# Performance work log

Measured on AMD Instinct MI355X. Metric: run time of the kernel, lower is better.

## Reference

```python
import jax, jax.numpy as jnp
import numpy as np

N_NODES = 100000


def _mean_agg(x, src, dst, n_nodes):
    # mean of src-node features over in-edges of each dst node (DGL copy_u + mean)
    summed = jax.ops.segment_sum(x[src], dst, num_segments=n_nodes)  # [N, F]
    deg = jax.ops.segment_sum(jnp.ones_like(src, dtype=x.dtype), dst, num_segments=n_nodes)
    return summed / jnp.maximum(deg, 1.0)[:, None]  # nodes w/o in-edges -> 0


def _sage_conv(x, src, dst, W_self, W_neigh, b):
    # DGL SAGEConv('mean'): fc_self(h) + fc_neigh(mean_neigh(h)) + bias
    h_neigh = _mean_agg(x, src, dst, x.shape[0])
    return x @ W_self + h_neigh @ W_neigh + b


def setup_inputs() -> dict:
    key = jax.random.key(0)
    ks = jax.random.split(key, 8)
    F_IN, F_H, E = 128, 128, 1600000
    s = 1.0 / np.sqrt(F_IN)
    return {
        "x": jax.random.normal(ks[0], (N_NODES, F_IN), dtype=jnp.float32),
        "src": jax.random.randint(ks[1], (E,), 0, N_NODES, dtype=jnp.int64),
        "dst": jax.random.randint(ks[2], (E,), 0, N_NODES, dtype=jnp.int64),
        "W1_self": jax.random.normal(ks[3], (F_IN, F_H), dtype=jnp.float32) * s,
        "W1_neigh": jax.random.normal(ks[4], (F_IN, F_H), dtype=jnp.float32) * s,
        "b1": jnp.zeros((F_H,), dtype=jnp.float32),
        "W2_self": jax.random.normal(ks[5], (F_H, F_H), dtype=jnp.float32) * s,
        "W2_neigh": jax.random.normal(ks[6], (F_H, F_H), dtype=jnp.float32) * s,
        "b2": jnp.zeros((F_H,), dtype=jnp.float32),
    }


def reference(x, src, dst, W1_self, W1_neigh, b1, W2_self, W2_neigh, b2):
    h = _sage_conv(x, src, dst, W1_self, W1_neigh, b1)
    # dropout in eval mode == identity
    h = jax.nn.relu(h)
    return _sage_conv(h, src, dst, W2_self, W2_neigh, b2)
```

## Files before the change

### kernel.cpp

```cpp
#include <hip/hip_runtime.h>

#define F 128
#define NN 100000
#define NBUK 782
#define NBLK 256
#define LD 136
#define N4 (NN * F / 4)
#define N4A (N4 / 2)
#define SORT_CAP 8192

typedef __attribute__((ext_vector_type(8))) short short8;
typedef __attribute__((ext_vector_type(4))) float f32x4;
typedef __attribute__((ext_vector_type(4))) int int4v;
typedef __attribute__((ext_vector_type(4))) unsigned short us4;
typedef unsigned short ushort_t;

__device__ __forceinline__ ushort_t f2b(float f) {
    union { float f; unsigned u; } x;
    x.f = f;
    unsigned r = x.u + 0x7fffu + ((x.u >> 16) & 1u);
    return (ushort_t)(r >> 16);
}
__device__ __forceinline__ float b2f(ushort_t u) {
    union { unsigned u; float f; } x;
    x.u = ((unsigned)u) << 16;
    return x.f;
}

__device__ __forceinline__ int4v ld_row16(const ushort_t* p) {
    int4v r;
    asm volatile("global_load_dwordx4 %0, %1, off" : "=v"(r) : "v"(p) : "memory");
    return r;
}

__global__ __launch_bounds__(256) void k1_fused(
    const int* __restrict__ dst, int* __restrict__ H, int E, int chunk,
    const float* __restrict__ Wa, const float* __restrict__ Wb,
    const float* __restrict__ Wc, const float* __restrict__ Wd,
    ushort_t* __restrict__ Oa, ushort_t* __restrict__ Ob,
    ushort_t* __restrict__ Oc, ushort_t* __restrict__ Od,
    const float* __restrict__ X, ushort_t* __restrict__ Y) {
    __shared__ union {
        int h[NBUK];
        float tile[32][33];
    } u;
    const int blk = blockIdx.x;
    if (blk < NBLK) {
        for (int i = threadIdx.x; i < NBUK; i += 256) u.h[i] = 0;
        __syncthreads();
        const int s0 = blk * chunk, s1 = min(E, s0 + chunk);
        for (int i = s0 + threadIdx.x; i < s1; i += 256)
            atomicAdd(&u.h[dst[i] >> 7], 1);
        __syncthreads();
        for (int i = threadIdx.x; i < NBUK; i += 256)
            H[blk * NBUK + i] = u.h[i];
    } else if (blk < NBLK + 64) {
        const int m = (blk - NBLK) >> 4;
        const int b = (blk - NBLK) & 15;
        const float* W = (m == 0) ? Wa : (m == 1) ? Wb : (m == 2) ? Wc : Wd;
        ushort_t* WT = (m == 0) ? Oa : (m == 1) ? Ob : (m == 2) ? Oc : Od;
        const int by = (b >> 2) * 32;
        const int bx = (b & 3) * 32;
        const int tx = threadIdx.x & 31, ty = threadIdx.x >> 5;
        for (int i = 0; i < 32; i += 8)
            u.tile[ty + i][tx] = W[(by + ty + i) * F + bx + tx];
        __syncthreads();
        for (int i = 0; i < 32; i += 8)
            WT[(bx + ty + i) * F + by + tx] = f2b(u.tile[tx][ty + i]);
    } else {
        const int i = (blk - NBLK - 64) * 256 + threadIdx.x;
        if (i < N4A) {
            float4 v = ((const float4*)X)[i];
            us4 o;
            o.x = f2b(v.x); o.y = f2b(v.y); o.z = f2b(v.z); o.w = f2b(v.w);
            ((us4*)Y)[i] = o;
        }
    }
}

__global__ __launch_bounds__(256) void scan_cols(int* __restrict__ H,
                                                 int* __restrict__ Htot) {
    __shared__ int s[NBLK];
    const int k = blockIdx.x;
    const int t = threadIdx.x;
    const int v = H[t * NBUK + k];
    s[t] = v;
    __syncthreads();
    for (int d = 1; d < NBLK; d <<= 1) {
        const int u = (t >= d) ? s[t - d] : 0;
        __syncthreads();
        s[t] += u;
        __syncthreads();
    }
    H[t * NBUK + k] = s[t] - v;
    if (t == NBLK - 1) Htot[k] = s[t];
}

__global__ __launch_bounds__(1024) void k2_fused(
    const int* __restrict__ Htot, int* __restrict__ boffs, int E,
    const float* __restrict__ X, ushort_t* __restrict__ Y) {
    if (blockIdx.x == 0) {
        __shared__ int tot[1024];
        const int k = threadIdx.x;
        const int v = (k < NBUK) ? Htot[k] : 0;
        tot[k] = v;
        __syncthreads();
        for (int d = 1; d < 1024; d <<= 1) {
            const int u = (k >= d) ? tot[k - d] : 0;
            __syncthreads();
            tot[k] += u;
            __syncthreads();
        }
        if (k < NBUK) boffs[k] = tot[k] - v;
        if (k == 0) boffs[NBUK] = E;
    } else {
        const int i = N4A + (blockIdx.x - 1) * 1024 + threadIdx.x;
        if (i < N4) {
            float4 v = ((const float4*)X)[i];
            us4 o;
            o.x = f2b(v.x); o.y = f2b(v.y); o.z = f2b(v.z); o.w = f2b(v.w);
            ((us4*)Y)[i] = o;
        }
    }
}

__global__ __launch_bounds__(256) void scatter2(const int* __restrict__ src,
                                                const int* __restrict__ dst,
                                                const int* __restrict__ H,
                                                const int* __restrict__ boffs,
                                                unsigned* __restrict__ pairs,
                                                int E, int chunk) {
    __shared__ int cur[NBUK];
    const int b = blockIdx.x;
    for (int i = threadIdx.x; i < NBUK; i += 256)
        cur[i] = boffs[i] + H[b * NBUK + i];
    __syncthreads();
    const int s0 = b * chunk, s1 = min(E, s0 + chunk);
    for (int i = s0 + threadIdx.x; i < s1; i += 256) {
        const int d = dst[i];
        const int p = atomicAdd(&cur[d >> 7], 1);
        pairs[p] = ((unsigned)(d & 127) << 20) | (unsigned)src[i];
    }
}

__global__ __launch_bounds__(256) void bucket_sort(const unsigned* __restrict__ pairs,
                                                   const int* __restrict__ boffs,
                                                   int* __restrict__ offs,
                                                   int* __restrict__ csr) {
    __shared__ int cnt[128], loffs[128], lcur[128];
    __shared__ unsigned sbuf[SORT_CAP];
    const int b = blockIdx.x, t = threadIdx.x;
    const int e0 = boffs[b], e1 = boffs[b + 1];
    const int n = e1 - e0;
    const int node0 = b << 7;
    const int nnode = min(128, NN - node0);
    if (t < 128) cnt[t] = 0;
    __syncthreads();
    for (int i = e0 + t; i < e1; i += 256) atomicAdd(&cnt[pairs[i] >> 20], 1);
    __syncthreads();
    if (t < 128) loffs[t] = cnt[t];
    __syncthreads();
    for (int d = 1; d < 128; d <<= 1) {
        int u = (t >= d && t < 128) ? loffs[t - d] : 0;
        __syncthreads();
        if (t < 128) loffs[t] += u;
        __syncthreads();
    }
    if (t < 128) {
        const int ex = loffs[t] - cnt[t];
        lcur[t] = ex;
        if (t < nnode) offs[node0 + t] = e0 + ex;
    }
    if (b == NBUK - 1 && t == 0) offs[NN] = e1;
    __syncthreads();

    if (n <= SORT_CAP) {
        for (int i = e0 + t; i < e1; i += 256) {
            const unsigned v = pairs[i];
            const int p = atomicAdd(&lcur[v >> 20], 1);
            sbuf[p] = v;
        }
        __syncthreads();
        for (int i = t; i < n; i += 256) {
            const unsigned v = sbuf[i];
            const int d = v >> 20;
            const int hi = loffs[d];
            const int lo = hi - cnt[d];
            int r = lo;
            for (int j = lo; j < hi; ++j) {
                const unsigned w = sbuf[j];
                r += (w < v) || (w == v && j < i);
            }
            csr[e0 + r] = (int)(v & 0xFFFFFu);
        }
    } else {
        for (int i = e0 + t; i < e1; i += 256) {
            const unsigned v = pairs[i];
            const int p = atomicAdd(&lcur[v >> 20], 1);
            csr[e0 + p] = (int)(v & 0xFFFFFu);
        }
    }
}

template <typename TOUT>
__global__ __launch_bounds__(256) void sage_layer(
    const ushort_t* __restrict__ Xg,
    const int* __restrict__ offs, const int* __restrict__ csr,
    const ushort_t* __restrict__ WTs, const ushort_t* __restrict__ WTn,
    const float* __restrict__ bias,
    TOUT* __restrict__ out, int relu) {
    __shared__ __align__(16) ushort_t sX[32 * LD];
    __shared__ __align__(16) ushort_t sH[32 * LD];
    const int t = threadIdx.x;
    const int lane = t & 63;
    const int wave = t >> 6;
    const int brow0 = blockIdx.x * 32;

    {
        const ushort_t* base = Xg + (size_t)brow0 * F;
        for (int i = t; i < 32 * 16; i += 256) {
            int row = i >> 4, ch = i & 15;
            *(short8*)&sX[row * LD + ch * 8] = *(const short8*)&base[row * F + ch * 8];
        }
    }

    {
        const int slot = lane >> 4;
        const int cl = lane & 15;
        const int c8 = cl * 8;
#pragma unroll
        for (int rr = 0; rr < 2; rr++) {
            const int rloc = wave * 8 + slot * 2 + rr;
            const int row = brow0 + rloc;
            const int e0 = offs[row], e1 = offs[row + 1];
            const int d = e1 - e0;
            float acc[8];
#pragma unroll
            for (int j = 0; j < 8; j++) acc[j] = 0.f;
            if (d > 0) {
                const int e1m1 = e1 - 1;
                const int nb = (d + 7) >> 3;
#pragma unroll 1
                for (int b = 0; b < nb; b++) {
                    const int e = e0 + b * 8;
                    const int i0 = csr[e];
                    const int i1 = csr[min(e + 1, e1m1)];
                    const int i2 = csr[min(e + 2, e1m1)];
                    const int i3 = csr[min(e + 3, e1m1)];
                    const int i4 = csr[min(e + 4, e1m1)];
                    const int i5 = csr[min(e + 5, e1m1)];
                    const int i6 = csr[min(e + 6, e1m1)];
                    const int i7 = csr[min(e + 7, e1m1)];
                    int4v r0 = ld_row16(Xg + (size_t)i0 * F + c8);
                    int4v r1 = ld_row16(Xg + (size_t)i1 * F + c8);
                    int4v r2 = ld_row16(Xg + (size_t)i2 * F + c8);
                    int4v r3 = ld_row16(Xg + (size_t)i3 * F + c8);
                    int4v r4 = ld_row16(Xg + (size_t)i4 * F + c8);
                    int4v r5 = ld_row16(Xg + (size_t)i5 * F + c8);
                    int4v r6 = ld_row16(Xg + (size_t)i6 * F + c8);
                    int4v r7 = ld_row16(Xg + (size_t)i7 * F + c8);
                    asm volatile("s_waitcnt vmcnt(0)" ::: "memory");
                    asm volatile("" : "+v"(r0), "+v"(r1), "+v"(r2), "+v"(r3),
                                       "+v"(r4), "+v"(r5), "+v"(r6), "+v"(r7));
                    __builtin_amdgcn_sched_barrier(0);
                    const short8 v0 = __builtin_bit_cast(short8, r0);
                    const short8 v1 = __builtin_bit_cast(short8, r1);
                    const short8 v2 = __builtin_bit_cast(short8, r2);
                    const short8 v3 = __builtin_bit_cast(short8, r3);
                    const short8 v4 = __builtin_bit_cast(short8, r4);
                    const short8 v5 = __builtin_bit_cast(short8, r5);
                    const short8 v6 = __builtin_bit_cast(short8, r6);
                    const short8 v7 = __builtin_bit_cast(short8, r7);
                    const float m1 = (e + 1 < e1) ? 1.f : 0.f;
                    const float m2 = (e + 2 < e1) ? 1.f : 0.f;
                    const float m3 = (e + 3 < e1) ? 1.f : 0.f;
                    const float m4 = (e + 4 < e1) ? 1.f : 0.f;
                    const float m5 = (e + 5 < e1) ? 1.f : 0.f;
                    const float m6 = (e + 6 < e1) ? 1.f : 0.f;
                    const float m7 = (e + 7 < e1) ? 1.f : 0.f;
#pragma unroll
                    for (int j = 0; j < 8; j++) {
                        float s01 = b2f((ushort_t)v0[j]) + m1 * b2f((ushort_t)v1[j]);
                        float s23 = m2 * b2f((ushort_t)v2[j]) + m3 * b2f((ushort_t)v3[j]);
                        float s45 = m4 * b2f((ushort_t)v4[j]) + m5 * b2f((ushort_t)v5[j]);
                        float s67 = m6 * b2f((ushort_t)v6[j]) + m7 * b2f((ushort_t)v7[j]);
                        acc[j] += (s01 + s23) + (s45 + s67);
                    }
                }
            }
            const float inv = (d > 0) ? (1.0f / (float)d) : 0.f;
            short8 o;
#pragma unroll
            for (int j = 0; j < 8; j++) o[j] = (short)f2b(acc[j] * inv);
            *(short8*)&sH[rloc * LD + c8] = o;
        }
    }
    __syncthreads();

    const int q = lane >> 4, nl = lane & 15;
    const int colbase = wave * 32;
    f32x4 acc00 = (f32x4)0.f, acc01 = (f32x4)0.f, acc10 = (f32x4)0.f, acc11 = (f32x4)0.f;
#pragma unroll
    for (int ks = 0; ks < 4; ks++) {
        const int ko = ks * 32 + q * 8;
        const short8 aS0 = *(const short8*)&sX[nl * LD + ko];
        const short8 aS1 = *(const short8*)&sX[(16 + nl) * LD + ko];
        const short8 aN0 = *(const short8*)&sH[nl * LD + ko];
        const short8 aN1 = *(const short8*)&sH[(16 + nl) * LD + ko];
        const size_t bo0 = (size_t)(colbase + nl) * F + ko;
        const size_t bo1 = (size_t)(colbase + 16 + nl) * F + ko;
        const short8 bS0 = *(const short8*)&WTs[bo0];
        const short8 bS1 = *(const short8*)&WTs[bo1];
        const short8 bN0 = *(const short8*)&WTn[bo0];
        const short8 bN1 = *(const short8*)&WTn[bo1];
        acc00 = __builtin_amdgcn_mfma_f32_16x16x32_bf16(aS0, bS0, acc00, 0, 0, 0);
        acc00 = __builtin_amdgcn_mfma_f32_16x16x32_bf16(aN0, bN0, acc00, 0, 0, 0);
        acc01 = __builtin_amdgcn_mfma_f32_16x16x32_bf16(aS0, bS1, acc01, 0, 0, 0);
        acc01 = __builtin_amdgcn_mfma_f32_16x16x32_bf16(aN0, bN1, acc01, 0, 0, 0);
        acc10 = __builtin_amdgcn_mfma_f32_16x16x32_bf16(aS1, bS0, acc10, 0, 0, 0);
        acc10 = __builtin_amdgcn_mfma_f32_16x16x32_bf16(aN1, bN0, acc10, 0, 0, 0);
        acc11 = __builtin_amdgcn_mfma_f32_16x16x32_bf16(aS1, bS1, acc11, 0, 0, 0);
        acc11 = __builtin_amdgcn_mfma_f32_16x16x32_bf16(aN1, bN1, acc11, 0, 0, 0);
    }

    const float b0 = bias[colbase + nl];
    const float b1 = bias[colbase + 16 + nl];
    if constexpr (sizeof(TOUT) == 2) {
        __syncthreads();
#pragma unroll
        for (int r = 0; r < 4; r++) {
            const int lr0 = q * 4 + r, lr1 = 16 + q * 4 + r;
            float v00 = acc00[r] + b0, v01 = acc01[r] + b1;
            float v10 = acc10[r] + b0, v11 = acc11[r] + b1;
            if (relu) {
                v00 = fmaxf(v00, 0.f); v01 = fmaxf(v01, 0.f);
                v10 = fmaxf(v10, 0.f); v11 = fmaxf(v11, 0.f);
            }
            sX[lr0 * LD + colbase + nl] = f2b(v00);
            sX[lr0 * LD + colbase + 16 + nl] = f2b(v01);
            sX[lr1 * LD + colbase + nl] = f2b(v10);
            sX[lr1 * LD + colbase + 16 + nl] = f2b(v11);
        }
        __syncthreads();
        TOUT* base = out + (size_t)brow0 * F;
        for (int i = t; i < 32 * 16; i += 256) {
            int row = i >> 4, ch = i & 15;
            *(short8*)&base[row * F + ch * 8] = *(const short8*)&sX[row * LD + ch * 8];
        }
    } else {
#pragma unroll
        for (int r = 0; r < 4; r++) {
            const int orow0 = brow0 + q * 4 + r;
            const int orow1 = brow0 + 16 + q * 4 + r;
            float v00 = acc00[r] + b0, v01 = acc01[r] + b1;
            float v10 = acc10[r] + b0, v11 = acc11[r] + b1;
            if (relu) {
                v00 = fmaxf(v00, 0.f); v01 = fmaxf(v01, 0.f);
                v10 = fmaxf(v10, 0.f); v11 = fmaxf(v11, 0.f);
            }
            out[(size_t)orow0 * F + colbase + nl] = v00;
            out[(size_t)orow0 * F + colbase + 16 + nl] = v01;
            out[(size_t)orow1 * F + colbase + nl] = v10;
            out[(size_t)orow1 * F + colbase + 16 + nl] = v11;
        }
    }
}

extern "C" void kernel_launch(void* const* d_in, const int* in_sizes, int n_in,
                              void* d_out, int out_size, void* d_ws, size_t ws_size,
                              hipStream_t stream) {
    const float* x = (const float*)d_in[0];
    const int* src = (const int*)d_in[1];
    const int* dst = (const int*)d_in[2];
    const float* W1s = (const float*)d_in[3];
    const float* W1n = (const float*)d_in[4];
    const float* b1 = (const float*)d_in[5];
    const float* W2s = (const float*)d_in[6];
    const float* W2n = (const float*)d_in[7];
    const float* b2 = (const float*)d_in[8];
    float* out = (float*)d_out;

    const int E = in_sizes[1];
    const int N = NN;
    const int E4 = (E + 3) & ~3;
    const int chunk = (E + NBLK - 1) / NBLK;

    unsigned* pairs = (unsigned*)d_ws;
    int* csr = (int*)(pairs + E4);
    ushort_t* h1 = (ushort_t*)(csr + E4);
    ushort_t* WT1s = h1 + (size_t)N * F;
    ushort_t* WT1n = WT1s + F * F;
    ushort_t* WT2s = WT1n + F * F;
    ushort_t* WT2n = WT2s + F * F;
    int* offs = (int*)(WT2n + F * F);
    int* H = offs + (N + 1);
    int* boffs = H + NBLK * NBUK;
    int* Htot = boffs + (NBUK + 1);
    ushort_t* xb = (ushort_t*)d_out;

    const int cvtA_blocks = (N4A + 255) / 256;
    k1_fused<<<NBLK + 64 + cvtA_blocks, 256, 0, stream>>>(
        dst, H, E, chunk, W1s, W1n, W2s, W2n, WT1s, WT1n, WT2s, WT2n, x, xb);
    scan_cols<<<NBUK, NBLK, 0, stream>>>(H, Htot);
    const int cvtB_blocks = (N4 - N4A + 1023) / 1024;
    k2_fused<<<1 + cvtB_blocks, 1024, 0, stream>>>(Htot, boffs, E, x, xb);
    scatter2<<<NBLK, 256, 0, stream>>>(src, dst, H, boffs, pairs, E, chunk);
    bucket_sort<<<NBUK, 256, 0, stream>>>(pairs, boffs, offs, csr);

    sage_layer<ushort_t><<<N / 32, 256, 0, stream>>>(
        xb, offs, csr, WT1s, WT1n, b1, h1, 1);
    sage_layer<float><<<N / 32, 256, 0, stream>>>(
        h1, offs, csr, WT2s, WT2n, b2, out, 0);
}
```

Before: 338.5 us.

## Gather neighbor features in FP8 e4m3 instead of bf16 for mean aggregation

Adds an FP8 (e4m3) copy of the input features and of the layer-1 output, and switches the neighbor gather in both SAGE layers to 8-byte FP8 row loads with 16 edges per batch. This halves the bytes fetched by the random-access gather, which dominates the aggregation cost. In exchange it does extra conversion work and writes, and it loses a lot of precision in the neighbor mean, which may break the accuracy tolerance. Layer 2 falls back to bf16 when the workspace is too small.

```diff
diff --git a/kernel.cpp b/kernel.cpp
--- a/kernel.cpp
+++ b/kernel.cpp
@@ -11,9 +11,12 @@
 
 typedef __attribute__((ext_vector_type(8))) short short8;
 typedef __attribute__((ext_vector_type(4))) float f32x4;
+typedef __attribute__((ext_vector_type(2))) float f32x2;
 typedef __attribute__((ext_vector_type(4))) int int4v;
+typedef __attribute__((ext_vector_type(2))) int int2v;
 typedef __attribute__((ext_vector_type(4))) unsigned short us4;
 typedef unsigned short ushort_t;
+typedef unsigned char uchar_t;
 
 __device__ __forceinline__ ushort_t f2b(float f) {
     union { float f; unsigned u; } x;
@@ -27,9 +30,59 @@
     return x.f;
 }
 
+__device__ __forceinline__ unsigned f_to_e4m3(float v) {
+    union { float f; unsigned b; } x; x.f = v;
+    unsigned s = (x.b >> 24) & 0x80u;
+    float a = fabsf(v);
+    if (!(a < 448.f)) return s | 0x7Eu;
+    if (a < 0.015625f) return s | (unsigned)__float2int_rn(a * 512.f);
+    unsigned ab = x.b & 0x7FFFFFFFu;
+    unsigned r = ab + 0x7FFFFu + ((ab >> 20) & 1u);
+    unsigned e = (r >> 23) - 120u;
+    return s | ((e << 3) | ((r >> 20) & 7u));
+}
+__device__ __forceinline__ float e4m3_to_f(unsigned u) {
+    unsigned s = (u & 0x80u) << 24;
+    unsigned e = (u >> 3) & 15u;
+    unsigned m = u & 7u;
+    union { unsigned b; float f; } x;
+    x.b = s | ((e + 120u) << 23) | (m << 20);
+    float f = x.f;
+    if (e == 0) f = fmaf(f, 2.f, s ? 0.015625f : -0.015625f);
+    return f;
+}
+__device__ __forceinline__ unsigned pack4_fp8(float f0, float f1, float f2, float f3) {
+#if __has_builtin(__builtin_amdgcn_cvt_pk_fp8_f32)
+    int w = 0;
+    w = __builtin_amdgcn_cvt_pk_fp8_f32(f0, f1, w, false);
+    w = __builtin_amdgcn_cvt_pk_fp8_f32(f2, f3, w, true);
+    return (unsigned)w;
+#else
+    return f_to_e4m3(f0) | (f_to_e4m3(f1) << 8) | (f_to_e4m3(f2) << 16) |
+           (f_to_e4m3(f3) << 24);
+#endif
+}
+__device__ __forceinline__ void dec4(int w, float* o) {
+#if __has_builtin(__builtin_amdgcn_cvt_pk_f32_fp8)
+    f32x2 a = __builtin_amdgcn_cvt_pk_f32_fp8(w, false);
+    f32x2 b = __builtin_amdgcn_cvt_pk_f32_fp8(w, true);
+    o[0] = a[0]; o[1] = a[1]; o[2] = b[0]; o[3] = b[1];
+#else
+    o[0] = e4m3_to_f((unsigned)w & 0xFFu);
+    o[1] = e4m3_to_f(((unsigned)w >> 8) & 0xFFu);
+    o[2] = e4m3_to_f(((unsigned)w >> 16) & 0xFFu);
+    o[3] = e4m3_to_f(((unsigned)w >> 24) & 0xFFu);
+#endif
+}
+
 __device__ __forceinline__ int4v ld_row16(const ushort_t* p) {
     int4v r;
     asm volatile("global_load_dwordx4 %0, %1, off" : "=v"(r) : "v"(p) : "memory");
+    return r;
+}
+__device__ __forceinline__ int2v ld_row8(const uchar_t* p) {
+    int2v r;
+    asm volatile("global_load_dwordx2 %0, %1, off" : "=v"(r) : "v"(p) : "memory");
     return r;
 }
 
@@ -39,7 +92,8 @@
     const float* __restrict__ Wc, const float* __restrict__ Wd,
     ushort_t* __restrict__ Oa, ushort_t* __restrict__ Ob,
     ushort_t* __restrict__ Oc, ushort_t* __restrict__ Od,
-    const float* __restrict__ X, ushort_t* __restrict__ Y) {
+    const float* __restrict__ X, ushort_t* __restrict__ Y,
+    uchar_t* __restrict__ X8) {
     __shared__ union {
         int h[NBUK];
         float tile[32][33];
@@ -74,6 +128,7 @@
             us4 o;
             o.x = f2b(v.x); o.y = f2b(v.y); o.z = f2b(v.z); o.w = f2b(v.w);
             ((us4*)Y)[i] = o;
+            ((unsigned*)X8)[i] = pack4_fp8(v.x, v.y, v.z, v.w);
         }
     }
 }
@@ -98,7 +153,8 @@
 
 __global__ __launch_bounds__(1024) void k2_fused(
     const int* __restrict__ Htot, int* __restrict__ boffs, int E,
-    const float* __restrict__ X, ushort_t* __restrict__ Y) {
+    const float* __restrict__ X, ushort_t* __restrict__ Y,
+    uchar_t* __restrict__ X8) {
     if (blockIdx.x == 0) {
         __shared__ int tot[1024];
         const int k = threadIdx.x;
@@ -120,6 +176,7 @@
             us4 o;
             o.x = f2b(v.x); o.y = f2b(v.y); o.z = f2b(v.z); o.w = f2b(v.w);
             ((us4*)Y)[i] = o;
+            ((unsigned*)X8)[i] = pack4_fp8(v.x, v.y, v.z, v.w);
         }
     }
 }
@@ -202,13 +259,13 @@
     }
 }
 
-template <typename TOUT>
+template <typename TOUT, int GF8>
 __global__ __launch_bounds__(256) void sage_layer(
-    const ushort_t* __restrict__ Xg,
+    const ushort_t* __restrict__ Xg, const uchar_t* __restrict__ X8g,
     const int* __restrict__ offs, const int* __restrict__ csr,
     const ushort_t* __restrict__ WTs, const ushort_t* __restrict__ WTn,
     const float* __restrict__ bias,
-    TOUT* __restrict__ out, int relu) {
+    TOUT* __restrict__ out, uchar_t* __restrict__ out8, int relu) {
     __shared__ __align__(16) ushort_t sX[32 * LD];
     __shared__ __align__(16) ushort_t sH[32 * LD];
     const int t = threadIdx.x;
@@ -239,52 +296,81 @@
             for (int j = 0; j < 8; j++) acc[j] = 0.f;
             if (d > 0) {
                 const int e1m1 = e1 - 1;
-                const int nb = (d + 7) >> 3;
+                if constexpr (GF8) {
+                    const int nb = (d + 15) >> 4;
 #pragma unroll 1
-                for (int b = 0; b < nb; b++) {
-                    const int e = e0 + b * 8;
-                    const int i0 = csr[e];
-                    const int i1 = csr[min(e + 1, e1m1)];
-                    const int i2 = csr[min(e + 2, e1m1)];
-                    const int i3 = csr[min(e + 3, e1m1)];
-                    const int i4 = csr[min(e + 4, e1m1)];
-                    const int i5 = csr[min(e + 5, e1m1)];
-                    const int i6 = csr[min(e + 6, e1m1)];
-                    const int i7 = csr[min(e + 7, e1m1)];
-                    int4v r0 = ld_row16(Xg + (size_t)i0 * F + c8);
-                    int4v r1 = ld_row16(Xg + (size_t)i1 * F + c8);
-                    int4v r2 = ld_row16(Xg + (size_t)i2 * F + c8);
-                    int4v r3 = ld_row16(Xg + (size_t)i3 * F + c8);
-                    int4v r4 = ld_row16(Xg + (size_t)i4 * F + c8);
-                    int4v r5 = ld_row16(Xg + (size_t)i5 * F + c8);
-                    int4v r6 = ld_row16(Xg + (size_t)i6 * F + c8);
-                    int4v r7 = ld_row16(Xg + (size_t)i7 * F + c8);
-                    asm volatile("s_waitcnt vmcnt(0)" ::: "memory");
-                    asm volatile("" : "+v"(r0), "+v"(r1), "+v"(r2), "+v"(r3),
-                                       "+v"(r4), "+v"(r5), "+v"(r6), "+v"(r7));
-                    __builtin_amdgcn_sched_barrier(0);
-                    const short8 v0 = __builtin_bit_cast(short8, r0);
-                    const short8 v1 = __builtin_bit_cast(short8, r1);
-                    const short8 v2 = __builtin_bit_cast(short8, r2);
-                    const short8 v3 = __builtin_bit_cast(short8, r3);
-                    const short8 v4 = __builtin_bit_cast(short8, r4);
-                    const short8 v5 = __builtin_bit_cast(short8, r5);
-                    const short8 v6 = __builtin_bit_cast(short8, r6);
-                    const short8 v7 = __builtin_bit_cast(short8, r7);
-                    const float m1 = (e + 1 < e1) ? 1.f : 0.f;
-                    const float m2 = (e + 2 < e1) ? 1.f : 0.f;
-                    const float m3 = (e + 3 < e1) ? 1.f : 0.f;
-                    const float m4 = (e + 4 < e1) ? 1.f : 0.f;
-                    const float m5 = (e + 5 < e1) ? 1.f : 0.f;
-                    const float m6 = (e + 6 < e1) ? 1.f : 0.f;
-                    const float m7 = (e + 7 < e1) ? 1.f : 0.f;
-#pragma unroll
-                    for (int j = 0; j < 8; j++) {
-                        float s01 = b2f((ushort_t)v0[j]) + m1 * b2f((ushort_t)v1[j]);
-                        float s23 = m2 * b2f((ushort_t)v2[j]) + m3 * b2f((ushort_t)v3[j]);
-                        float s45 = m4 * b2f((ushort_t)v4[j]) + m5 * b2f((ushort_t)v5[j]);
-                        float s67 = m6 * b2f((ushort_t)v6[j]) + m7 * b2f((ushort_t)v7[j]);
-                        acc[j] += (s01 + s23) + (s45 + s67);
+                    for (int b = 0; b < nb; b++) {
+                        const int e = e0 + b * 16;
+#define IDX9(K) const int i##K = csr[min(e + K, e1m1)];
+                        IDX9(0) IDX9(1) IDX9(2) IDX9(3) IDX9(4) IDX9(5) IDX9(6) IDX9(7)
+                        IDX9(8) IDX9(9) IDX9(10) IDX9(11) IDX9(12) IDX9(13) IDX9(14) IDX9(15)
+#undef IDX9
+#define LDR9(K) int2v r##K = ld_row8(X8g + (size_t)i##K * F + c8);
+                        LDR9(0) LDR9(1) LDR9(2) LDR9(3) LDR9(4) LDR9(5) LDR9(6) LDR9(7)
+                        LDR9(8) LDR9(9) LDR9(10) LDR9(11) LDR9(12) LDR9(13) LDR9(14) LDR9(15)
+#undef LDR9
+                        asm volatile("s_waitcnt vmcnt(0)" ::: "memory");
+                        asm volatile("" : "+v"(r0), "+v"(r1), "+v"(r2), "+v"(r3),
+                                           "+v"(r4), "+v"(r5), "+v"(r6), "+v"(r7),
+                                           "+v"(r8), "+v"(r9), "+v"(r10), "+v"(r11),
+                                           "+v"(r12), "+v"(r13), "+v"(r14), "+v"(r15));
+                        __builtin_amdgcn_sched_barrier(0);
+#define ACC9(K) { float tv[8]; dec4(r##K.x, tv); dec4(r##K.y, tv + 4);            \
+                  const float mk = (e + K < e1) ? 1.f : 0.f;                      \
+                  _Pragma("unroll")                                               \
+                  for (int j = 0; j < 8; j++) acc[j] = fmaf(mk, tv[j], acc[j]); }
+                        ACC9(0) ACC9(1) ACC9(2) ACC9(3) ACC9(4) ACC9(5) ACC9(6) ACC9(7)
+                        ACC9(8) ACC9(9) ACC9(10) ACC9(11) ACC9(12) ACC9(13) ACC9(14) ACC9(15)
+#undef ACC9
+                    }
+                } else {
+                    const int nb = (d + 7) >> 3;
+#pragma unroll 1
+                    for (int b = 0; b < nb; b++) {
+                        const int e = e0 + b * 8;
+                        const int i0 = csr[e];
+                        const int i1 = csr[min(e + 1, e1m1)];
+                        const int i2 = csr[min(e + 2, e1m1)];
+                        const int i3 = csr[min(e + 3, e1m1)];
+                        const int i4 = csr[min(e + 4, e1m1)];
+                        const int i5 = csr[min(e + 5, e1m1)];
+                        const int i6 = csr[min(e + 6, e1m1)];
+                        const int i7 = csr[min(e + 7, e1m1)];
+                        int4v r0 = ld_row16(Xg + (size_t)i0 * F + c8);
+                        int4v r1 = ld_row16(Xg + (size_t)i1 * F + c8);
+                        int4v r2 = ld_row16(Xg + (size_t)i2 * F + c8);
+                        int4v r3 = ld_row16(Xg + (size_t)i3 * F + c8);
+                        int4v r4 = ld_row16(Xg + (size_t)i4 * F + c8);
+                        int4v r5 = ld_row16(Xg + (size_t)i5 * F + c8);
+                        int4v r6 = ld_row16(Xg + (size_t)i6 * F + c8);
+                        int4v r7 = ld_row16(Xg + (size_t)i7 * F + c8);
+                        asm volatile("s_waitcnt vmcnt(0)" ::: "memory");
+                        asm volatile("" : "+v"(r0), "+v"(r1), "+v"(r2), "+v"(r3),
+                                           "+v"(r4), "+v"(r5), "+v"(r6), "+v"(r7));
+                        __builtin_amdgcn_sched_barrier(0);
+                        const short8 v0 = __builtin_bit_cast(short8, r0);
+                        const short8 v1 = __builtin_bit_cast(short8, r1);
+                        const short8 v2 = __builtin_bit_cast(short8, r2);
+                        const short8 v3 = __builtin_bit_cast(short8, r3);
+                        const short8 v4 = __builtin_bit_cast(short8, r4);
+                        const short8 v5 = __builtin_bit_cast(short8, r5);
+                        const short8 v6 = __builtin_bit_cast(short8, r6);
+                        const short8 v7 = __builtin_bit_cast(short8, r7);
+                        const float m1 = (e + 1 < e1) ? 1.f : 0.f;
+                        const float m2 = (e + 2 < e1) ? 1.f : 0.f;
+                        const float m3 = (e + 3 < e1) ? 1.f : 0.f;
+                        const float m4 = (e + 4 < e1) ? 1.f : 0.f;
+                        const float m5 = (e + 5 < e1) ? 1.f : 0.f;
+                        const float m6 = (e + 6 < e1) ? 1.f : 0.f;
+                        const float m7 = (e + 7 < e1) ? 1.f : 0.f;
+#pragma unroll
+                        for (int j = 0; j < 8; j++) {
+                            float s01 = b2f((ushort_t)v0[j]) + m1 * b2f((ushort_t)v1[j]);
+                            float s23 = m2 * b2f((ushort_t)v2[j]) + m3 * b2f((ushort_t)v3[j]);
+                            float s45 = m4 * b2f((ushort_t)v4[j]) + m5 * b2f((ushort_t)v5[j]);
+                            float s67 = m6 * b2f((ushort_t)v6[j]) + m7 * b2f((ushort_t)v7[j]);
+                            acc[j] += (s01 + s23) + (s45 + s67);
+                        }
                     }
                 }
             }
@@ -345,7 +431,17 @@
         TOUT* base = out + (size_t)brow0 * F;
         for (int i = t; i < 32 * 16; i += 256) {
             int row = i >> 4, ch = i & 15;
-            *(short8*)&base[row * F + ch * 8] = *(const short8*)&sX[row * LD + ch * 8];
+            const short8 v = *(const short8*)&sX[row * LD + ch * 8];
+            *(short8*)&base[row * F + ch * 8] = v;
+            if (out8) {
+                float f[8];
+#pragma unroll
+                for (int j = 0; j < 8; j++) f[j] = b2f((ushort_t)v[j]);
+                int2v p;
+                p.x = (int)pack4_fp8(f[0], f[1], f[2], f[3]);
+                p.y = (int)pack4_fp8(f[4], f[5], f[6], f[7]);
+                *(int2v*)&out8[(size_t)(brow0 + row) * F + ch * 8] = p;
+            }
         }
     } else {
 #pragma unroll
@@ -397,18 +493,28 @@
     int* boffs = H + NBLK * NBUK;
     int* Htot = boffs + (NBUK + 1);
     ushort_t* xb = (ushort_t*)d_out;
+    uchar_t* x8 = (uchar_t*)d_out + (size_t)N * F * 2;
+    size_t off8 = (size_t)((char*)(Htot + NBUK) - (char*)d_ws);
+    off8 = (off8 + 7) & ~(size_t)7;
+    uchar_t* h1f8 = (uchar_t*)d_ws + off8;
+    const bool l2f8 = ws_size >= off8 + (size_t)N * F;
 
     const int cvtA_blocks = (N4A + 255) / 256;
     k1_fused<<<NBLK + 64 + cvtA_blocks, 256, 0, stream>>>(
-        dst, H, E, chunk, W1s, W1n, W2s, W2n, WT1s, WT1n, WT2s, WT2n, x, xb);
+        dst, H, E, chunk, W1s, W1n, W2s, W2n, WT1s, WT1n, WT2s, WT2n, x, xb, x8);
     scan_cols<<<NBUK, NBLK, 0, stream>>>(H, Htot);
     const int cvtB_blocks = (N4 - N4A + 1023) / 1024;
-    k2_fused<<<1 + cvtB_blocks, 1024, 0, stream>>>(Htot, boffs, E, x, xb);
+    k2_fused<<<1 + cvtB_blocks, 1024, 0, stream>>>(Htot, boffs, E, x, xb, x8);
     scatter2<<<NBLK, 256, 0, stream>>>(src, dst, H, boffs, pairs, E, chunk);
     bucket_sort<<<NBUK, 256, 0, stream>>>(pairs, boffs, offs, csr);
 
-    sage_layer<ushort_t><<<N / 32, 256, 0, stream>>>(
-        xb, offs, csr, WT1s, WT1n, b1, h1, 1);
-    sage_layer<float><<<N / 32, 256, 0, stream>>>(
-        h1, offs, csr, WT2s, WT2n, b2, out, 0);
-}
+    sage_layer<ushort_t, 1><<<N / 32, 256, 0, stream>>>(
+        xb, x8, offs, csr, WT1s, WT1n, b1, h1, l2f8 ? h1f8 : nullptr, 1);
+    if (l2f8) {
+        sage_layer<float, 1><<<N / 32, 256, 0, stream>>>(
+            h1, h1f8, offs, csr, WT2s, WT2n, b2, out, nullptr, 0);
+    } else {
+        sage_layer<float, 0><<<N / 32, 256, 0, stream>>>(
+            h1, nullptr, offs, csr, WT2s, WT2n, b2, out, nullptr, 0);
+    }
+}
```

New measurement: 334.6 us. About the same (-1.2%).
